# Kernel tuning notes

Hardware: AMD Instinct MI355X
Metric: run time of the kernel (lower is better)

The kernel has to match this reference:

```python
import jax, jax.numpy as jnp
import numpy as np
import math

B, T, D, H = 4, 2048, 1024, 16
HD = D // H  # head dim = 64
ROPE_BASE = 10000.0


def apply_rope(x):
    # x: [b, h, t, hd]. Positions start at 1 (seq_id = arange(1, t+1)) per the source.
    t, hd = x.shape[2], x.shape[3]
    half = hd // 2
    theta = 1.0 / (ROPE_BASE ** (jnp.arange(0, hd, 2, dtype=jnp.float32) / hd))  # [hd/2]
    pos = jnp.arange(1, t + 1, dtype=jnp.float32)  # [t]
    ang = pos[:, None] * theta[None, :]             # [t, hd/2]
    ang = jnp.concatenate([ang, ang], axis=-1)      # [t, hd]
    sin, cos = jnp.sin(ang), jnp.cos(ang)
    # rotate-half: cat([-x2, x1])
    rot = jnp.concatenate([-x[..., half:], x[..., :half]], axis=-1)
    return x * cos[None, None, :, :] + rot * sin[None, None, :, :]


def setup_inputs() -> dict:
    key = jax.random.key(0)
    ks = jax.random.split(key, 9)
    s = 1.0 / math.sqrt(D)
    return {
        "x": jax.random.normal(ks[0], (B, T, D), dtype=jnp.float32),
        "Wq": jax.random.normal(ks[1], (D, D), dtype=jnp.float32) * s,
        "bq": jax.random.normal(ks[2], (D,), dtype=jnp.float32) * 0.01,
        "Wk": jax.random.normal(ks[3], (D, D), dtype=jnp.float32) * s,
        "bk": jax.random.normal(ks[4], (D,), dtype=jnp.float32) * 0.01,
        "Wv": jax.random.normal(ks[5], (D, D), dtype=jnp.float32) * s,
        "bv": jax.random.normal(ks[6], (D,), dtype=jnp.float32) * 0.01,
        "Wo": jax.random.normal(ks[7], (D, D), dtype=jnp.float32) * s,
        "bo": jax.random.normal(ks[8], (D,), dtype=jnp.float32) * 0.01,
    }


def reference(x, Wq, bq, Wk, bk, Wv, bv, Wo, bo):
    b, t, d = x.shape
    h, hd = H, HD
    # projections (torch Linear: x @ W.T + b)
    q = x @ Wq.T + bq
    k = x @ Wk.T + bk
    v = x @ Wv.T + bv
    # [b, t, d] -> [b, h, t, hd]
    split = lambda z: z.reshape(b, t, h, hd).transpose(0, 2, 1, 3)
    q, k, v = split(q), split(k), split(v)
    q = apply_rope(q)
    k = apply_rope(k)
    scale = math.sqrt(hd)
    att = jnp.einsum('bhqd,bhkd->bhqk', q, k) / scale
    mask = jnp.tril(jnp.ones((t, t), dtype=bool))
    att = jnp.where(mask[None, None, :, :], att, -jnp.inf)
    att = jax.nn.softmax(att, axis=-1)
    y = jnp.einsum('bhqk,bhkd->bhqd', att, v)
    y = y.transpose(0, 2, 1, 3).reshape(b, t, d)
    y = y @ Wo.T + bo
    return y
```

## Files before the change

kernel.cpp:

```cpp
#include <hip/hip_runtime.h>

#define BB 4
#define TT 2048
#define DD 1024
#define HH 16
#define HD 64

typedef __attribute__((ext_vector_type(8))) _Float16 f16x8;
typedef __attribute__((ext_vector_type(4))) float f32x4;
typedef __attribute__((ext_vector_type(2))) unsigned int u32x2;
typedef __attribute__((ext_vector_type(4))) unsigned int u32x4;

__device__ __forceinline__ float h2f(unsigned short u) {
    return (float)__builtin_bit_cast(_Float16, u);
}
__device__ __forceinline__ unsigned short f2h(float f) {
    return __builtin_bit_cast(unsigned short, (_Float16)f);
}
__device__ __forceinline__ unsigned int pkrtz(float a, float b) {
    return __builtin_bit_cast(unsigned int, __builtin_amdgcn_cvt_pkrtz(a, b));
}

__global__ __launch_bounds__(256) void conv_all(
    const float4* __restrict__ x,
    const float4* __restrict__ Wq, const float4* __restrict__ Wk,
    const float4* __restrict__ Wv,
    ushort4* __restrict__ xh, ushort4* __restrict__ wh,
    float2* __restrict__ tab)
{
    int vi = blockIdx.x * 256 + threadIdx.x;
    if (vi < 2097152) {
        float4 v = x[vi];
        xh[vi] = (ushort4){ f2h(v.x), f2h(v.y), f2h(v.z), f2h(v.w) };
    } else if (vi < 2883584) {
        int u = vi - 2097152;
        int w = u >> 18;
        const float4* src = (w == 0) ? Wq : (w == 1) ? Wk : Wv;
        float4 v = src[u & 262143];
        wh[u] = (ushort4){ f2h(v.x), f2h(v.y), f2h(v.z), f2h(v.w) };
    } else {
        int u = vi - 2883584;
        int t = u >> 5, i = u & 31;
        float ang = (float)(t + 1) *
                    exp2f(-(float)i * (13.287712379549449f / 32.0f));
        tab[u] = (float2){ cosf(ang), sinf(ang) };
    }
}

__global__ __launch_bounds__(256) void conv_wo(
    const float4* __restrict__ Wo, ushort4* __restrict__ dst)
{
    int i = blockIdx.x * 256 + threadIdx.x;
    float4 v = Wo[i];
    dst[i] = (ushort4){ f2h(v.x), f2h(v.y), f2h(v.z), f2h(v.w) };
}

#define GLDS(gp, lp)                                                          \
    __builtin_amdgcn_global_load_lds(                                         \
        (const __attribute__((address_space(1))) unsigned int*)(gp),          \
        (__attribute__((address_space(3))) unsigned int*)(lp), 16, 0, 0)

__global__ __launch_bounds__(256) void gemm_qkv(
    const unsigned short* __restrict__ A,
    const unsigned short* __restrict__ Wall,
    const float* __restrict__ bq, const float* __restrict__ bk,
    const float* __restrict__ bv,
    const float2* __restrict__ tab,
    unsigned short* __restrict__ qkv)
{
    __shared__ __align__(16) unsigned short As[2 * 128 * 64];
    __shared__ __align__(16) unsigned short Ws[2 * 128 * 64];

    int bid = blockIdx.x;
    int swz = (bid & 7) * 192 + (bid >> 3);
    int bx = swz % 24, by = swz / 24;
    const int sel = bx >> 3;
    const int jb = bx & 7;
    const int n0 = by * 128;
    const int j0 = jb * 128;

    const unsigned short* W = Wall + (size_t)sel * 1048576;
    const float* bias = (sel == 0) ? bq : (sel == 1) ? bk : bv;
    unsigned short* outp = qkv + (size_t)sel * (BB * HH * TT * HD);

    const int tid = threadIdx.x;
    const int w = tid >> 6, lane = tid & 63;
    const int l15 = lane & 15, g = lane >> 4;
    const int wr = w >> 1, wc = w & 1;
    const int wavebase = tid & ~63;

    f32x4 acc[4][4];
#pragma unroll
    for (int mi = 0; mi < 4; mi++)
#pragma unroll
        for (int nj = 0; nj < 4; nj++) acc[mi][nj] = (f32x4){0.f, 0.f, 0.f, 0.f};

#define ISSUE(KS, BUF)                                                        \
    {                                                                         \
        _Pragma("unroll")                                                     \
        for (int it = 0; it < 4; it++) {                                      \
            int ci = it * 256 + tid;                                          \
            int r = ci >> 3;                                                  \
            int p = (ci & 7) ^ (r & 7);                                       \
            int lb = (BUF) * 8192 + (it * 256 + wavebase) * 8;                \
            GLDS(A + (size_t)(n0 + r) * 1024 + (KS) + p * 8, As + lb);        \
            GLDS(W + (size_t)(j0 + r) * 1024 + (KS) + p * 8, Ws + lb);        \
        }                                                                     \
    }

    ISSUE(0, 0)
    ISSUE(64, 1)

    for (int ki = 0; ki < 16; ki++) {
        const int cur = ki & 1;
        if (ki < 15) asm volatile("s_waitcnt vmcnt(8)" ::: "memory");
        else         asm volatile("s_waitcnt vmcnt(0)" ::: "memory");
        __builtin_amdgcn_s_barrier();
        const unsigned short* Ab = As + cur * 8192;
        const unsigned short* Wb = Ws + cur * 8192;

#pragma unroll
        for (int c = 0; c < 2; c++) {
            f16x8 af[4], bf[4];
            const int q0c = c * 4 + (g >> 1);
            const int q1c = q0c + 2;
            const int off = (g & 1) << 2;
#pragma unroll
            for (int mi = 0; mi < 4; mi++) {
                int r = wr * 64 + mi * 16 + l15;
                int sw = r & 7;
                const unsigned short* rp = Ab + r * 64;
                u32x2 x0 = *(const u32x2*)(rp + ((q0c ^ sw) << 3) + off);
                u32x2 x1 = *(const u32x2*)(rp + ((q1c ^ sw) << 3) + off);
                u32x4 uu = {x0.x, x0.y, x1.x, x1.y};
                af[mi] = __builtin_bit_cast(f16x8, uu);
            }
#pragma unroll
            for (int nj = 0; nj < 4; nj++) {
                int r = wc * 64 + nj * 16 + l15;
                int sw = r & 7;
                const unsigned short* rp = Wb + r * 64;
                u32x2 x0 = *(const u32x2*)(rp + ((q0c ^ sw) << 3) + off);
                u32x2 x1 = *(const u32x2*)(rp + ((q1c ^ sw) << 3) + off);
                u32x4 uu = {x0.x, x0.y, x1.x, x1.y};
                bf[nj] = __builtin_bit_cast(f16x8, uu);
            }
#pragma unroll
            for (int mi = 0; mi < 4; mi++)
#pragma unroll
                for (int nj = 0; nj < 4; nj++)
                    acc[mi][nj] = __builtin_amdgcn_mfma_f32_16x16x32_f16(
                        af[mi], bf[nj], acc[mi][nj], 0, 0, 0);
        }

        __builtin_amdgcn_s_barrier();
        if (ki + 2 < 16) ISSUE((ki + 2) * 64, cur)
    }
#undef ISSUE

    float bb4[4];
#pragma unroll
    for (int nj = 0; nj < 4; nj++) bb4[nj] = bias[j0 + wc * 64 + nj * 16 + l15];
    const int hh = (j0 >> 6) + wc;

    if (sel == 2) {
#pragma unroll
        for (int mi = 0; mi < 4; mi++)
#pragma unroll
            for (int r = 0; r < 4; r++) {
                int n = n0 + wr * 64 + mi * 16 + 4 * g + r;
                int b = n >> 11, t = n & (TT - 1);
                size_t rowbase = ((size_t)(b * HH + hh) * TT + t) << 6;
#pragma unroll
                for (int nj = 0; nj < 4; nj++) {
                    int dd = nj * 16 + l15;
                    outp[rowbase + dd] = f2h(acc[mi][nj][r] + bb4[nj]);
                }
            }
    } else {
#pragma unroll
        for (int mi = 0; mi < 4; mi++)
#pragma unroll
            for (int r = 0; r < 4; r++) {
                int n = n0 + wr * 64 + mi * 16 + 4 * g + r;
                int b = n >> 11, t = n & (TT - 1);
                size_t rowbase = ((size_t)(b * HH + hh) * TT + t) << 6;
                const float2* tp = tab + t * 32 + l15;
#pragma unroll
                for (int p = 0; p < 2; p++) {
                    float2 cs = tp[p * 16];
                    float x1 = acc[mi][p][r]     + bb4[p];
                    float x2 = acc[mi][p + 2][r] + bb4[p + 2];
                    int i = p * 16 + l15;
                    outp[rowbase + i]      = f2h(x1 * cs.x - x2 * cs.y);
                    outp[rowbase + i + 32] = f2h(x2 * cs.x + x1 * cs.y);
                }
            }
    }
}

__global__ __launch_bounds__(256) void gemm_h(
    const unsigned short* __restrict__ A, const unsigned short* __restrict__ W,
    const float* __restrict__ bias, float* __restrict__ outp,
    int N, int K, int J)
{
    __shared__ __align__(16) unsigned short As[2 * 128 * 64];
    __shared__ __align__(16) unsigned short Ws[2 * 128 * 64];

    int total = gridDim.x * gridDim.y;
    int flat = blockIdx.y * gridDim.x + blockIdx.x;
    int swz = (flat & 7) * (total >> 3) + (flat >> 3);
    int bxi = swz % gridDim.x, byi = swz / gridDim.x;

    const int tid = threadIdx.x;
    const int w = tid >> 6, lane = tid & 63;
    const int l15 = lane & 15, g = lane >> 4;
    const int wr = w >> 1, wc = w & 1;
    const int n0 = byi * 128;
    const int j0 = bxi * 128;
    const int wavebase = tid & ~63;

    f32x4 acc[4][4];
#pragma unroll
    for (int mi = 0; mi < 4; mi++)
#pragma unroll
        for (int nj = 0; nj < 4; nj++) acc[mi][nj] = (f32x4){0.f, 0.f, 0.f, 0.f};

#define ISSUE(KS, BUF)                                                        \
    {                                                                         \
        _Pragma("unroll")                                                     \
        for (int it = 0; it < 4; it++) {                                      \
            int ci = it * 256 + tid;                                          \
            int r = ci >> 3;                                                  \
            int p = (ci & 7) ^ (r & 7);                                       \
            int lb = (BUF) * 8192 + (it * 256 + wavebase) * 8;                \
            GLDS(A + (size_t)(n0 + r) * K + (KS) + p * 8, As + lb);           \
            GLDS(W + (size_t)(j0 + r) * K + (KS) + p * 8, Ws + lb);           \
        }                                                                     \
    }

    const int nks = K >> 6;
    ISSUE(0, 0)
    if (nks > 1) ISSUE(64, 1)

    for (int ki = 0; ki < nks; ki++) {
        const int cur = ki & 1;
        if (ki < nks - 1) asm volatile("s_waitcnt vmcnt(8)" ::: "memory");
        else              asm volatile("s_waitcnt vmcnt(0)" ::: "memory");
        __builtin_amdgcn_s_barrier();
        const unsigned short* Ab = As + cur * 8192;
        const unsigned short* Wb = Ws + cur * 8192;

#pragma unroll
        for (int c = 0; c < 2; c++) {
            f16x8 af[4], bf[4];
            const int q0c = c * 4 + (g >> 1);
            const int q1c = q0c + 2;
            const int off = (g & 1) << 2;
#pragma unroll
            for (int mi = 0; mi < 4; mi++) {
                int r = wr * 64 + mi * 16 + l15;
                int sw = r & 7;
                const unsigned short* rp = Ab + r * 64;
                u32x2 x0 = *(const u32x2*)(rp + ((q0c ^ sw) << 3) + off);
                u32x2 x1 = *(const u32x2*)(rp + ((q1c ^ sw) << 3) + off);
                u32x4 uu = {x0.x, x0.y, x1.x, x1.y};
                af[mi] = __builtin_bit_cast(f16x8, uu);
            }
#pragma unroll
            for (int nj = 0; nj < 4; nj++) {
                int r = wc * 64 + nj * 16 + l15;
                int sw = r & 7;
                const unsigned short* rp = Wb + r * 64;
                u32x2 x0 = *(const u32x2*)(rp + ((q0c ^ sw) << 3) + off);
                u32x2 x1 = *(const u32x2*)(rp + ((q1c ^ sw) << 3) + off);
                u32x4 uu = {x0.x, x0.y, x1.x, x1.y};
                bf[nj] = __builtin_bit_cast(f16x8, uu);
            }
#pragma unroll
            for (int mi = 0; mi < 4; mi++)
#pragma unroll
                for (int nj = 0; nj < 4; nj++)
                    acc[mi][nj] = __builtin_amdgcn_mfma_f32_16x16x32_f16(
                        af[mi], bf[nj], acc[mi][nj], 0, 0, 0);
        }

        __builtin_amdgcn_s_barrier();
        if (ki + 2 < nks) ISSUE((ki + 2) * 64, cur)
    }
#undef ISSUE

#pragma unroll
    for (int nj = 0; nj < 4; nj++) {
        int j = j0 + wc * 64 + nj * 16 + l15;
        float bb = bias[j];
#pragma unroll
        for (int mi = 0; mi < 4; mi++)
#pragma unroll
            for (int r = 0; r < 4; r++) {
                int n = n0 + wr * 64 + mi * 16 + 4 * g + r;
                outp[(size_t)n * J + j] = acc[mi][nj][r] + bb;
            }
    }
}

__device__ __forceinline__ u32x2 ds_tr16(const unsigned short* p) {
    u32x2 r;
    asm volatile("ds_read_b64_tr_b16 %0, %1"
                 : "=v"(r)
                 : "v"((unsigned int)(unsigned long long)p));
    return r;
}

__global__ __launch_bounds__(512, 4) void attn_mfma(
    const unsigned short* __restrict__ q,
    const unsigned short* __restrict__ k,
    const unsigned short* __restrict__ v,
    unsigned short* __restrict__ aout)
{
    __shared__ __align__(16) unsigned short Ks[64 * 64];
    __shared__ __align__(16) unsigned short Vs[4 * 1056];

    const int h = blockIdx.y, b = blockIdx.z;
    const int tid = threadIdx.x;
    const int w = tid >> 6;
    const int wd = w & 3;
    const int wt = w >> 2;
    const int lane = tid & 63;
    const int l15 = lane & 15, g = lane >> 4;
    const int bh = b * HH + h;
    const size_t base = (size_t)bh * TT * 64;
    const unsigned short* Qp = q + base;
    const unsigned short* Kp = k + base;
    const unsigned short* Vp = v + base;

    const float SC = 0.18033688011112042f;

    u32x4 kreg;
    u32x2 vreg[2];
#define LOADKV(KB)                                                             \
    {                                                                          \
        {                                                                      \
            int key = tid >> 3, pr = tid & 7;                                  \
            kreg = *(const u32x4*)(Kp + (size_t)((KB) + key) * 64 + pr * 8);   \
        }                                                                      \
        _Pragma("unroll")                                                      \
        for (int it = 0; it < 2; it++) {                                       \
            int vi = tid + it * 512;                                           \
            int key = vi >> 4, c4 = vi & 15;                                   \
            vreg[it] = *(const u32x2*)(Vp + (size_t)((KB) + key) * 64 + c4 * 4);\
        }                                                                      \
    }

    for (int ph = 0; ph < 2; ph++) {
        const int qs = ph ? (15 - (int)blockIdx.x) : (int)blockIdx.x;
        const int q0 = qs * 128;
        const int dtile = 2 * qs + wt;

        f16x8 qf[2];
        {
            const unsigned short* Qr = Qp + (size_t)(q0 + w * 16 + l15) * 64;
#pragma unroll
            for (int c = 0; c < 2; c++) {
                u32x2 a0 = *(const u32x2*)(Qr + 32 * c + 4 * g);
                u32x2 a1 = *(const u32x2*)(Qr + 32 * c + 16 + 4 * g);
                u32x4 uu = {a0.x, a0.y, a1.x, a1.y};
                qf[c] = __builtin_bit_cast(f16x8, uu);
            }
        }

        float mrow = -1e30f, lrow = 0.f;
        f32x4 accO[4];
#pragma unroll
        for (int nb = 0; nb < 4; nb++) accO[nb] = (f32x4){0.f, 0.f, 0.f, 0.f};

        const int ntiles = 2 * qs + 2;
        LOADKV(0)

        for (int kt = 0; kt < ntiles; kt++) {
            const bool active = (kt <= dtile);
            const bool diag = (kt == dtile);
            __syncthreads();
            {
                int key = tid >> 3, pr = tid & 7;
                *(u32x4*)(Ks + key * 64 + ((pr ^ (key & 7)) << 3)) = kreg;
            }
#pragma unroll
            for (int it = 0; it < 2; it++) {
                int vi = tid + it * 512;
                int key = vi >> 4, c4 = vi & 15;
                *(u32x2*)(Vs + (c4 >> 2) * 1056 + key * 16 + (c4 & 3) * 4) = vreg[it];
            }
            __syncthreads();
            if (kt + 1 < ntiles) LOADKV((kt + 1) * 64)

            if (active) {
                const int nkb = diag ? (wd + 1) : 4;
                f32x4 accS[4];
#pragma unroll
                for (int kb = 0; kb < 4; kb++) accS[kb] = (f32x4){0.f, 0.f, 0.f, 0.f};
                __builtin_amdgcn_s_setprio(1);
#pragma unroll
                for (int kb = 0; kb < 4; kb++) {
                    if (kb < nkb) {
                        int key = kb * 16 + l15;
                        int sw = key & 7;
#pragma unroll
                        for (int c = 0; c < 2; c++) {
                            int c8a = 8 * c + g, c8b = 8 * c + 4 + g;
                            u32x2 x0 = *(const u32x2*)(Ks + key * 64 +
                                           (((c8a >> 1) ^ sw) << 3) + ((c8a & 1) << 2));
                            u32x2 x1 = *(const u32x2*)(Ks + key * 64 +
                                           (((c8b >> 1) ^ sw) << 3) + ((c8b & 1) << 2));
                            u32x4 uu = {x0.x, x0.y, x1.x, x1.y};
                            accS[kb] = __builtin_amdgcn_mfma_f32_16x16x32_f16(
                                __builtin_bit_cast(f16x8, uu), qf[c], accS[kb], 0, 0, 0);
                        }
                    }
                }
                __builtin_amdgcn_s_setprio(0);

                float sloc[16];
                float tmax = -1e30f;
                if (diag) {
#pragma unroll
                    for (int kb = 0; kb < 4; kb++)
#pragma unroll
                        for (int r = 0; r < 4; r++) {
                            float s = accS[kb][r];
                            bool valid = (kb * 16 + 4 * g + r <= wd * 16 + l15);
                            s = valid ? s : -1e30f;
                            sloc[kb * 4 + r] = s;
                            tmax = fmaxf(tmax, s);
                        }
                } else {
#pragma unroll
                    for (int kb = 0; kb < 4; kb++)
#pragma unroll
                        for (int r = 0; r < 4; r++) {
                            float s = accS[kb][r];
                            sloc[kb * 4 + r] = s;
                            tmax = fmaxf(tmax, s);
                        }
                }
                tmax = fmaxf(tmax, __shfl_xor(tmax, 16));
                tmax = fmaxf(tmax, __shfl_xor(tmax, 32));

                if (!__all(tmax - mrow <= 61.0f)) {
                    float mnew = fmaxf(mrow, tmax);
                    float sf = exp2f((mrow - mnew) * SC);
                    mrow = mnew;
                    lrow *= sf;
                    float sfr[4];
#pragma unroll
                    for (int r = 0; r < 4; r++) sfr[r] = __shfl(sf, 4 * g + r);
#pragma unroll
                    for (int nb = 0; nb < 4; nb++)
#pragma unroll
                        for (int r = 0; r < 4; r++) accO[nb][r] *= sfr[r];
                }

                const float nmsc = -mrow * SC;
                unsigned int pw[8];
                float psum = 0.f;
#pragma unroll
                for (int i = 0; i < 8; i++) {
                    float p0 = exp2f(fmaf(sloc[2 * i],     SC, nmsc));
                    float p1 = exp2f(fmaf(sloc[2 * i + 1], SC, nmsc));
                    pw[i] = pkrtz(p0, p1);
                    psum += p0 + p1;
                }
                psum += __shfl_xor(psum, 16);
                psum += __shfl_xor(psum, 32);
                lrow += psum;

                const int nkc = (diag && wd < 2) ? 1 : 2;
#pragma unroll
                for (int kc = 0; kc < 2; kc++)
                    if (kc < nkc) {
                        u32x2 vfr[4][2];
#pragma unroll
                        for (int nb = 0; nb < 4; nb++)
#pragma unroll
                            for (int t2 = 0; t2 < 2; t2++)
                                vfr[nb][t2] = ds_tr16(
                                    Vs + nb * 1056 + (kc * 32 + 16 * t2) * 16 + 4 * lane);
                        asm volatile("s_waitcnt lgkmcnt(0)" ::: "memory");
                        __builtin_amdgcn_sched_barrier(0);
                        u32x4 pu = {pw[4 * kc + 0], pw[4 * kc + 1], pw[4 * kc + 2], pw[4 * kc + 3]};
                        f16x8 pf = __builtin_bit_cast(f16x8, pu);
                        __builtin_amdgcn_s_setprio(1);
#pragma unroll
                        for (int nb = 0; nb < 4; nb++) {
                            u32x4 vu = {vfr[nb][0].x, vfr[nb][0].y,
                                        vfr[nb][1].x, vfr[nb][1].y};
                            accO[nb] = __builtin_amdgcn_mfma_f32_16x16x32_f16(
                                pf, __builtin_bit_cast(f16x8, vu), accO[nb], 0, 0, 0);
                        }
                        __builtin_amdgcn_s_setprio(0);
                    }
            }
        }

        float linv = 1.0f / lrow;
        float sfr[4];
#pragma unroll
        for (int r = 0; r < 4; r++) sfr[r] = __shfl(linv, 4 * g + r);
#pragma unroll
        for (int r = 0; r < 4; r++) {
            int qr = q0 + w * 16 + 4 * g + r;
            unsigned short* orow = aout + (size_t)(b * TT + qr) * DD + h * 64;
#pragma unroll
            for (int nb = 0; nb < 4; nb++)
                orow[nb * 16 + l15] = f2h(accO[nb][r] * sfr[r]);
        }
    }
#undef LOADKV
}

extern "C" void kernel_launch(void* const* d_in, const int* in_sizes, int n_in,
                              void* d_out, int out_size, void* d_ws, size_t ws_size,
                              hipStream_t stream)
{
    const float* x  = (const float*)d_in[0];
    const float* Wq = (const float*)d_in[1];
    const float* bq = (const float*)d_in[2];
    const float* Wk = (const float*)d_in[3];
    const float* bk = (const float*)d_in[4];
    const float* Wv = (const float*)d_in[5];
    const float* bv = (const float*)d_in[6];
    const float* Wo = (const float*)d_in[7];
    const float* bo = (const float*)d_in[8];
    float* out = (float*)d_out;

    const size_t NE = (size_t)BB * HH * TT * HD;
    unsigned short* qkv  = (unsigned short*)d_ws;
    unsigned short* qb   = qkv;
    unsigned short* kbuf = qkv + NE;
    unsigned short* vbuf = qkv + 2 * NE;
    float* res = (float*)d_ws;

    unsigned short* ds  = (unsigned short*)d_out;
    unsigned short* xh  = ds;
    unsigned short* wh  = ds + 8388608;
    float2* tab = (float2*)(ds + 11534336);

    const bool direct = ws_size >= (size_t)8 * NE;
    unsigned short* att = direct ? (qkv + 3 * NE) : ds;
    unsigned short* woh = direct ? (unsigned short*)d_ws : (ds + 11796480);
    float* resout = direct ? out : res;

    const int N = BB * TT;
    dim3 blk(256);

    conv_all<<<11520, blk, 0, stream>>>(
        (const float4*)x, (const float4*)Wq, (const float4*)Wk,
        (const float4*)Wv, (ushort4*)xh, (ushort4*)wh, tab);

    gemm_qkv<<<1536, blk, 0, stream>>>(xh, wh, bq, bk, bv, tab, qkv);

    attn_mfma<<<dim3(8, HH, BB), dim3(512), 0, stream>>>(qb, kbuf, vbuf, att);

    conv_wo<<<1024, blk, 0, stream>>>((const float4*)Wo, (ushort4*)woh);

    gemm_h<<<dim3(DD / 128, N / 128), blk, 0, stream>>>(att, woh, bo, resout, N, DD, DD);

    if (!direct)
        hipMemcpyAsync(out, res, (size_t)N * DD * sizeof(float),
                       hipMemcpyDeviceToDevice, stream);
}
```

Baseline: 276.4 us.

## Fold softmax scale into Q projection and compute row sums via MFMA

The softmax scale (1/sqrt(hd)·log2e) is now applied to Q in the projection epilogue, so the attention inner loop computes exp2(s - m) without a per-element FMA. The per-row probability sum is accumulated by an extra MFMA against a ones vector, replacing the scalar adds and cross-lane shuffles. The rescale threshold is lowered to match the new units. The cost is one extra MFMA per PV chunk. Scaling Q before the fp16 cast slightly changes rounding.

Measured after the change: 281.9 us. +2.0%, slower.

```diff
diff --git a/kernel.cpp b/kernel.cpp
--- a/kernel.cpp
+++ b/kernel.cpp
@@ -178,6 +178,7 @@
                 }
             }
     } else {
+        const float osc = (sel == 0) ? 0.18033688011112042f : 1.0f;
 #pragma unroll
         for (int mi = 0; mi < 4; mi++)
 #pragma unroll
@@ -192,8 +193,8 @@
                     float x1 = acc[mi][p][r]     + bb4[p];
                     float x2 = acc[mi][p + 2][r] + bb4[p + 2];
                     int i = p * 16 + l15;
-                    outp[rowbase + i]      = f2h(x1 * cs.x - x2 * cs.y);
-                    outp[rowbase + i + 32] = f2h(x2 * cs.x + x1 * cs.y);
+                    outp[rowbase + i]      = f2h((x1 * cs.x - x2 * cs.y) * osc);
+                    outp[rowbase + i + 32] = f2h((x2 * cs.x + x1 * cs.y) * osc);
                 }
             }
     }
@@ -334,7 +335,8 @@
     const unsigned short* Kp = k + base;
     const unsigned short* Vp = v + base;
 
-    const float SC = 0.18033688011112042f;
+    const u32x4 onesu = {0x3C003C00u, 0x3C003C00u, 0x3C003C00u, 0x3C003C00u};
+    const f16x8 onesf = __builtin_bit_cast(f16x8, onesu);
 
     u32x4 kreg;
     u32x2 vreg[2];
@@ -369,8 +371,9 @@
             }
         }
 
-        float mrow = -1e30f, lrow = 0.f;
+        float mrow = -1e30f;
         f32x4 accO[4];
+        f32x4 accL = (f32x4){0.f, 0.f, 0.f, 0.f};
 #pragma unroll
         for (int nb = 0; nb < 4; nb++) accO[nb] = (f32x4){0.f, 0.f, 0.f, 0.f};
 
@@ -446,33 +449,28 @@
                 tmax = fmaxf(tmax, __shfl_xor(tmax, 16));
                 tmax = fmaxf(tmax, __shfl_xor(tmax, 32));
 
-                if (!__all(tmax - mrow <= 61.0f)) {
+                if (!__all(tmax - mrow <= 11.0f)) {
                     float mnew = fmaxf(mrow, tmax);
-                    float sf = exp2f((mrow - mnew) * SC);
+                    float sf = exp2f(mrow - mnew);
                     mrow = mnew;
-                    lrow *= sf;
                     float sfr[4];
 #pragma unroll
                     for (int r = 0; r < 4; r++) sfr[r] = __shfl(sf, 4 * g + r);
+#pragma unroll
+                    for (int r = 0; r < 4; r++) accL[r] *= sfr[r];
 #pragma unroll
                     for (int nb = 0; nb < 4; nb++)
 #pragma unroll
                         for (int r = 0; r < 4; r++) accO[nb][r] *= sfr[r];
                 }
 
-                const float nmsc = -mrow * SC;
                 unsigned int pw[8];
-                float psum = 0.f;
 #pragma unroll
                 for (int i = 0; i < 8; i++) {
-                    float p0 = exp2f(fmaf(sloc[2 * i],     SC, nmsc));
-                    float p1 = exp2f(fmaf(sloc[2 * i + 1], SC, nmsc));
+                    float p0 = exp2f(sloc[2 * i]     - mrow);
+                    float p1 = exp2f(sloc[2 * i + 1] - mrow);
                     pw[i] = pkrtz(p0, p1);
-                    psum += p0 + p1;
                 }
-                psum += __shfl_xor(psum, 16);
-                psum += __shfl_xor(psum, 32);
-                lrow += psum;
 
                 const int nkc = (diag && wd < 2) ? 1 : 2;
 #pragma unroll
@@ -497,22 +495,21 @@
                             accO[nb] = __builtin_amdgcn_mfma_f32_16x16x32_f16(
                                 pf, __builtin_bit_cast(f16x8, vu), accO[nb], 0, 0, 0);
                         }
+                        accL = __builtin_amdgcn_mfma_f32_16x16x32_f16(
+                            pf, onesf, accL, 0, 0, 0);
                         __builtin_amdgcn_s_setprio(0);
                     }
             }
         }
 
-        float linv = 1.0f / lrow;
-        float sfr[4];
-#pragma unroll
-        for (int r = 0; r < 4; r++) sfr[r] = __shfl(linv, 4 * g + r);
 #pragma unroll
         for (int r = 0; r < 4; r++) {
+            float linv = 1.0f / accL[r];
             int qr = q0 + w * 16 + 4 * g + r;
             unsigned short* orow = aout + (size_t)(b * TT + qr) * DD + h * 64;
 #pragma unroll
             for (int nb = 0; nb < 4; nb++)
-                orow[nb * 16 + l15] = f2h(accO[nb][r] * sfr[r]);
+                orow[nb * 16 + l15] = f2h(accO[nb][r] * linv);
         }
     }
 #undef LOADKV
```
